# Kernel tuning notes

Measured on AMD Instinct MI355X. Metric: run time of the kernel, lower is better.

## Reference

```python
import jax, jax.numpy as jnp
import numpy as np

B, S, H, NH, FF = 8, 512, 1024, 16, 4096
DK = H // NH


def _ln(x, g, b):
    m = x.mean(-1, keepdims=True)
    v = ((x - m) ** 2).mean(-1, keepdims=True)
    return (x - m) / jnp.sqrt(v + 1e-5) * g + b


def _fwd(x, predicate_pos, attn_bias, attention_mask, atom_graph, variable_graph,
         ln1_g, ln1_b, wq, bq, wk, bk, wv, bv, wo, bo,
         pq_w, pq_b, pk_w, pk_b, pv_w, pv_b, ln2_g, ln2_b, w1, b1, w2, b2):
    b_, s_, h_ = x.shape
    y = _ln(x, ln1_g, ln1_b)
    # ---- self attention (manual MHA with additive bias + mask) ----
    scale = DK ** -0.5
    q = (y @ wq + bq).reshape(b_, s_, NH, DK) * scale
    k = (y @ wk + bk).reshape(b_, s_, NH, DK)
    v = (y @ wv + bv).reshape(b_, s_, NH, DK)
    scores = jnp.einsum('bihd,bjhd->bhij', q, k)
    scores = scores + attn_bias[:, None, :, :] + attention_mask[:, None, :, :]
    att = jax.nn.softmax(scores, axis=-1)
    y_self = jnp.einsum('bhij,bjhd->bihd', att, v).reshape(b_, s_, h_) @ wo + bo
    # ---- path attention (single-head with graph biases) ----
    pscale = h_ ** -0.5
    pq = (y @ pq_w + pq_b) * pscale
    pk = y @ pk_w + pk_b
    pv = y @ pv_w + pv_b
    patt = jnp.einsum('bid,bjd->bij', pq, pk) + atom_graph + variable_graph
    patt = jax.nn.softmax(patt, axis=-1)
    xp = jnp.einsum('bij,bjd->bid', patt, pv)  # [B,S,H]
    # vectorized gather-mean over predicate positions (replaces per-sample loop)
    prev = jnp.concatenate([xp[:, :1], xp[:, :-1]], axis=1)   # xp[i-1]
    nxt = jnp.concatenate([xp[:, 1:], xp[:, -1:]], axis=1)    # xp[i+1]
    a0 = xp[:, 0:2].mean(axis=1, keepdims=True)               # i == 0
    a1 = xp[:, 0:3].mean(axis=1, keepdims=True)               # i == 1
    a2 = (xp + nxt) / 2.0                                     # pos[i-2] == 1
    a3 = (prev + xp + nxt) / 3.0                              # else
    i_arr = jnp.arange(s_)
    pos = (predicate_pos == 1)
    pos_m2 = jnp.pad(pos[:, :-2], ((0, 0), (2, 0)))           # pos[i-2], False for i<2
    atom = jnp.where(pos_m2[..., None], a2, a3)
    atom = jnp.where((i_arr == 1)[None, :, None], a1, atom)
    atom = jnp.where((i_arr == 0)[None, :, None], a0, atom)
    w = pos.astype(xp.dtype)
    path = (atom * w[..., None]).sum(1) / w.sum(1, keepdims=True)  # [B,H]
    y_path = jnp.broadcast_to(path[:, None, :], (b_, s_, h_))
    # ---- combine + residual + FFN ----
    x = x + (y_self + y_path) / 2.0
    y2 = _ln(x, ln2_g, ln2_b)
    hmid = jax.nn.gelu(y2 @ w1 + b1, approximate=False)
    return x + (hmid @ w2 + b2)


def setup_inputs() -> dict:
    key = jax.random.key(0)
    ks = jax.random.split(key, 16)
    def w(k, shape):
        return 0.02 * jax.random.normal(k, shape, dtype=jnp.float32)
    pp = jax.random.randint(ks[0], (B, S), 0, 2, dtype=jnp.int32)
    pp = pp.at[:, 2].set(1).at[:, -1].set(0)  # >=1 predicate; no predicate at last node
    return {
        'x': jax.random.normal(ks[1], (B, S, H), dtype=jnp.float32),
        'predicate_pos': pp,
        'variable_tags': jnp.zeros((B, S), dtype=jnp.int32),
        'attn_bias': 0.1 * jax.random.normal(ks[2], (B, S, S), dtype=jnp.float32),
        'attention_mask': jnp.zeros((B, S, S), dtype=jnp.float32),
        'atom_graph': 0.1 * jax.random.normal(ks[3], (B, S, S), dtype=jnp.float32),
        'variable_graph': 0.1 * jax.random.normal(ks[4], (B, S, S), dtype=jnp.float32),
        'ln1_g': jnp.ones((H,), jnp.float32), 'ln1_b': jnp.zeros((H,), jnp.float32),
        'wq': w(ks[5], (H, H)), 'bq': jnp.zeros((H,), jnp.float32),
        'wk': w(ks[6], (H, H)), 'bk': jnp.zeros((H,), jnp.float32),
        'wv': w(ks[7], (H, H)), 'bv': jnp.zeros((H,), jnp.float32),
        'wo': w(ks[8], (H, H)), 'bo': jnp.zeros((H,), jnp.float32),
        'pq_w': w(ks[9], (H, H)), 'pq_b': jnp.zeros((H,), jnp.float32),
        'pk_w': w(ks[10], (H, H)), 'pk_b': jnp.zeros((H,), jnp.float32),
        'pv_w': w(ks[11], (H, H)), 'pv_b': jnp.zeros((H,), jnp.float32),
        'ln2_g': jnp.ones((H,), jnp.float32), 'ln2_b': jnp.zeros((H,), jnp.float32),
        'w1': w(ks[12], (H, FF)), 'b1': jnp.zeros((FF,), jnp.float32),
        'w2': w(ks[13], (FF, H)), 'b2': jnp.zeros((H,), jnp.float32),
    }


def reference(x, predicate_pos, variable_tags, attn_bias, attention_mask, atom_graph, variable_graph,
              ln1_g, ln1_b, wq, bq, wk, bk, wv, bv, wo, bo,
              pq_w, pq_b, pk_w, pk_b, pv_w, pv_b, ln2_g, ln2_b, w1, b1, w2, b2):
    # variable_tags is unused in the original forward as well
    return _fwd(x, predicate_pos, attn_bias, attention_mask, atom_graph, variable_graph,
                ln1_g, ln1_b, wq, bq, wk, bk, wv, bv, wo, bo,
                pq_w, pq_b, pk_w, pk_b, pv_w, pv_b, ln2_g, ln2_b, w1, b1, w2, b2)
```

## Files before the change

### kernel.cpp

```cpp
#include <hip/hip_runtime.h>
#include <hip/hip_bf16.h>
#include <math.h>


typedef __bf16 bf16x8 __attribute__((ext_vector_type(8)));
typedef float f32x4 __attribute__((ext_vector_type(4)));

__device__ __forceinline__ void async_copy16(void* lds, const void* g) {
  __builtin_amdgcn_global_load_lds(
      (__attribute__((address_space(1))) void*)(void*)g,
      (__attribute__((address_space(3))) void*)lds, 16, 0, 0);
}

#define SB0 __builtin_amdgcn_sched_barrier(0)
#define BARRIER __builtin_amdgcn_s_barrier()

__global__ __launch_bounds__(256) void ln_rows_bf16(
    const float* __restrict__ X, const float* __restrict__ G,
    const float* __restrict__ Bt, __hip_bfloat16* __restrict__ O) {
  long row = blockIdx.x;
  int t = threadIdx.x;
  const float4 xv = ((const float4*)(X + row * 1024))[t];
  float s = xv.x + xv.y + xv.z + xv.w;
  float q = xv.x * xv.x + xv.y * xv.y + xv.z * xv.z + xv.w * xv.w;
#pragma unroll
  for (int o = 32; o; o >>= 1) {
    s += __shfl_xor(s, o);
    q += __shfl_xor(q, o);
  }
  __shared__ float rs[4], rq[4];
  int wid = t >> 6;
  if ((t & 63) == 0) { rs[wid] = s; rq[wid] = q; }
  __syncthreads();
  s = rs[0] + rs[1] + rs[2] + rs[3];
  q = rq[0] + rq[1] + rq[2] + rq[3];
  float mean = s * (1.f / 1024.f);
  float var = q * (1.f / 1024.f) - mean * mean;
  float rstd = rsqrtf(var + 1e-5f);
  const float4 gv = ((const float4*)G)[t];
  const float4 bv = ((const float4*)Bt)[t];
  __hip_bfloat16* o = O + row * 1024 + t * 4;
  o[0] = __float2bfloat16((xv.x - mean) * rstd * gv.x + bv.x);
  o[1] = __float2bfloat16((xv.y - mean) * rstd * gv.y + bv.y);
  o[2] = __float2bfloat16((xv.z - mean) * rstd * gv.z + bv.z);
  o[3] = __float2bfloat16((xv.w - mean) * rstd * gv.w + bv.w);
}

struct PrepJobs {
  const float* in[15];
  __hip_bfloat16* out[15];
  int inLd[15];
  int outLd[15];
  float scale[15];
  const float* bsrc[6];
  float bscale[6];
  float* bias6;
  const float* lnx;
  const float* lng;
  const float* lnb;
  __hip_bfloat16* lno;
};
__global__ __launch_bounds__(256) void prep_weights(PrepJobs p) {
  int j = blockIdx.z;
  int tid = threadIdx.x;
  if (j >= 16) {
    long row = (long)(j - 16) * 1024 + blockIdx.y * 32 + blockIdx.x;
    const float4 xv = ((const float4*)(p.lnx + row * 1024))[tid];
    float s = xv.x + xv.y + xv.z + xv.w;
    float q = xv.x * xv.x + xv.y * xv.y + xv.z * xv.z + xv.w * xv.w;
#pragma unroll
    for (int o = 32; o; o >>= 1) {
      s += __shfl_xor(s, o);
      q += __shfl_xor(q, o);
    }
    __shared__ float rs[4], rq[4];
    int wid = tid >> 6;
    if ((tid & 63) == 0) { rs[wid] = s; rq[wid] = q; }
    __syncthreads();
    s = rs[0] + rs[1] + rs[2] + rs[3];
    q = rq[0] + rq[1] + rq[2] + rq[3];
    float mean = s * (1.f / 1024.f);
    float var = q * (1.f / 1024.f) - mean * mean;
    float rstd = rsqrtf(var + 1e-5f);
    const float4 gv = ((const float4*)p.lng)[tid];
    const float4 bv = ((const float4*)p.lnb)[tid];
    __hip_bfloat16* o = p.lno + row * 1024 + tid * 4;
    o[0] = __float2bfloat16((xv.x - mean) * rstd * gv.x + bv.x);
    o[1] = __float2bfloat16((xv.y - mean) * rstd * gv.y + bv.y);
    o[2] = __float2bfloat16((xv.z - mean) * rstd * gv.z + bv.z);
    o[3] = __float2bfloat16((xv.w - mean) * rstd * gv.w + bv.w);
    return;
  }
  if (j == 15) {
    if (blockIdx.y == 0 && blockIdx.x < 24) {
      int idx = blockIdx.x * 256 + tid;
      int jj = idx >> 10, e = idx & 1023;
      p.bias6[idx] = p.bsrc[jj][e] * p.bscale[jj];
    }
    return;
  }
  __shared__ float t[32][33];
  const float* in = p.in[j];
  __hip_bfloat16* out = p.out[j];
  const int inLd = p.inLd[j], outLd = p.outLd[j];
  const float sc = p.scale[j];
  int c0 = blockIdx.x * 32, r0 = blockIdx.y * 32;
  int lr = tid >> 3, lc = (tid & 7) * 4;
  const float4 v = *(const float4*)&in[(long)(r0 + lr) * inLd + c0 + lc];
  t[lr][lc] = v.x; t[lr][lc + 1] = v.y; t[lr][lc + 2] = v.z; t[lr][lc + 3] = v.w;
  __syncthreads();
  int oc = tid >> 3, orr = (tid & 7) * 4;
  __hip_bfloat16* o = &out[(long)(c0 + oc) * outLd + r0 + orr];
  o[0] = __float2bfloat16(t[orr][oc] * sc);
  o[1] = __float2bfloat16(t[orr + 1][oc] * sc);
  o[2] = __float2bfloat16(t[orr + 2][oc] * sc);
  o[3] = __float2bfloat16(t[orr + 3][oc] * sc);
}

__global__ __launch_bounds__(256) void tconv_vpv(
    const __hip_bfloat16* __restrict__ V, const __hip_bfloat16* __restrict__ PV,
    __hip_bfloat16* __restrict__ VT, __hip_bfloat16* __restrict__ PVT) {
  __shared__ __hip_bfloat16 t[32][34];
  int z = blockIdx.z;
  const __hip_bfloat16* in = (z < 8) ? V : PV;
  __hip_bfloat16* out = (z < 8) ? VT : PVT;
  int bz = z & 7;
  long ibase = (long)bz * 512 * 6144;
  long obase = (long)bz * 512 * 1024;
  int c0 = blockIdx.x * 32, r0 = blockIdx.y * 32;
  int tid = threadIdx.x;
  int lr = tid >> 3, lc = (tid & 7) * 4;
  const __hip_bfloat16* ip = &in[ibase + (long)(r0 + lr) * 6144 + c0 + lc];
  t[lr][lc] = ip[0]; t[lr][lc + 1] = ip[1]; t[lr][lc + 2] = ip[2]; t[lr][lc + 3] = ip[3];
  __syncthreads();
  int oc = tid >> 3, orr = (tid & 7) * 4;
  __hip_bfloat16* o = &out[obase + (long)(c0 + oc) * 512 + r0 + orr];
  o[0] = t[orr][oc];
  o[1] = t[orr + 1][oc];
  o[2] = t[orr + 2][oc];
  o[3] = t[orr + 3][oc];
}

__global__ __launch_bounds__(512, 2) void gemm256(
    const __hip_bfloat16* __restrict__ A, const __hip_bfloat16* __restrict__ Bt,
    const float* __restrict__ bias, void* __restrict__ C, int K, int lda,
    int ldb, int ldc, int act, int obf, long sC) {
  constexpr int ABYTES = 256 * 64;
  constexpr int BBYTES = 128 * 64;
  constexpr int BUF = ABYTES + BBYTES;
  __shared__ char lds[2 * BUF];

  int bx, by;
  {
    int wg = blockIdx.y * gridDim.x + blockIdx.x;
    int gx = gridDim.x, gy = gridDim.y;
    if ((gx & 3) == 0 && (gy & 1) == 0) {
      int cw = gx >> 2, ch = gy >> 1;
      int xcd = wg & 7, idx = wg >> 3;
      bx = (xcd & 3) * cw + idx % cw;
      by = (xcd >> 2) * ch + idx / cw;
    } else {
      bx = blockIdx.x;
      by = blockIdx.y;
    }
  }
  const int m0 = by * 256, n0 = bx * 128;
  const int z = blockIdx.z;
  const long kbase = (long)z * K * 2;

  const int tid = threadIdx.x;
  const int lane = tid & 63, wid = tid >> 6;
  const int wm = wid >> 2, wn = wid & 3;
  const int ll = lane & 15, lh = lane >> 4;

  const char* Ag = (const char*)A;
  const char* Bg = (const char*)Bt;
  const int srow = tid >> 2;
  const int ssw = (srow ^ (srow >> 2)) & 3;
  const int scb = (((tid & 3) ^ ssw) << 4);
  const int sld = (tid & 3) << 4;

  auto stage = [&](char* base, long kb) {
#pragma unroll
    for (int l = 0; l < 2; ++l) {
      int row = l * 128 + srow;
      async_copy16(base + row * 64 + sld,
                   Ag + ((long)(m0 + row) * lda) * 2 + kb + scb);
    }
    async_copy16(base + ABYTES + srow * 64 + sld,
                 Bg + ((long)(n0 + srow) * ldb) * 2 + kb + scb);
  };

  const int rsw = (ll ^ (ll >> 2)) & 3;
  const int ckk = ((lh ^ rsw) << 4);

  f32x4 acc[8][2];
#pragma unroll
  for (int m = 0; m < 8; ++m)
#pragma unroll
    for (int n = 0; n < 2; ++n) acc[m][n] = (f32x4){0.f, 0.f, 0.f, 0.f};

  const int nt = K >> 5;
  stage(lds, kbase);

  for (int t = 0; t < nt; ++t) {
    const int bt = t & 1;
    const char* Ab = lds + bt * BUF;
    const char* Bb = Ab + ABYTES;
    char* nb = lds + (bt ^ 1) * BUF;

    SB0; BARRIER; SB0;
    if (t + 1 < nt) {
      stage(nb, kbase + (long)(t + 1) * 64);
      asm volatile("s_waitcnt vmcnt(3)" ::: "memory");
    } else {
      asm volatile("s_waitcnt vmcnt(0)" ::: "memory");
    }
    SB0; BARRIER; SB0;

    bf16x8 bf[2];
#pragma unroll
    for (int n = 0; n < 2; ++n)
      bf[n] = *(const bf16x8*)(Bb + (wn * 32 + n * 16 + ll) * 64 + ckk);
    bf16x8 af[4];
#pragma unroll
    for (int m = 0; m < 4; ++m)
      af[m] = *(const bf16x8*)(Ab + (wm * 128 + m * 16 + ll) * 64 + ckk);
    __builtin_amdgcn_s_setprio(1);
#pragma unroll
    for (int m = 0; m < 4; ++m)
#pragma unroll
      for (int n = 0; n < 2; ++n)
        acc[m][n] = __builtin_amdgcn_mfma_f32_16x16x32_bf16(af[m], bf[n],
                                                            acc[m][n], 0, 0, 0);
    __builtin_amdgcn_s_setprio(0);
#pragma unroll
    for (int m = 0; m < 4; ++m)
      af[m] = *(const bf16x8*)(Ab + (wm * 128 + (m + 4) * 16 + ll) * 64 + ckk);
    __builtin_amdgcn_s_setprio(1);
#pragma unroll
    for (int m = 0; m < 4; ++m)
#pragma unroll
      for (int n = 0; n < 2; ++n)
        acc[m + 4][n] = __builtin_amdgcn_mfma_f32_16x16x32_bf16(
            af[m], bf[n], acc[m + 4][n], 0, 0, 0);
    __builtin_amdgcn_s_setprio(0);
  }

#pragma unroll
  for (int m = 0; m < 8; ++m) {
    int row = m0 + wm * 128 + m * 16 + lh * 4;
#pragma unroll
    for (int n = 0; n < 2; ++n) {
      int col = n0 + wn * 32 + n * 16 + ll;
      float bs = bias ? bias[col] : 0.f;
#pragma unroll
      for (int r = 0; r < 4; ++r) {
        float v = acc[m][n][r] + bs;
        if (act) v = v * 0.5f * (1.f + erff(v * 0.70710678118f));
        long cidx = (long)z * sC + (long)(row + r) * ldc + col;
        if (obf)
          ((__hip_bfloat16*)C)[cidx] = __float2bfloat16(v);
        else
          ((float*)C)[cidx] = v;
      }
    }
  }
}

__global__ __launch_bounds__(256) void ffn2_reduce(
    const float* __restrict__ P, const float* __restrict__ X2,
    const float* __restrict__ b2, float* __restrict__ OUT) {
  int i = blockIdx.x * 256 + threadIdx.x;
  const long SP = 4194304;
  float4 a = ((const float4*)P)[i];
  float4 b = ((const float4*)(P + SP))[i];
  float4 c = ((const float4*)(P + 2 * SP))[i];
  float4 d = ((const float4*)(P + 3 * SP))[i];
  float4 xr = ((const float4*)X2)[i];
  const float4 bb = *(const float4*)(b2 + ((i & 255) * 4));
  float4 o;
  o.x = a.x + b.x + c.x + d.x + xr.x + bb.x;
  o.y = a.y + b.y + c.y + d.y + xr.y + bb.y;
  o.z = a.z + b.z + c.z + d.z + xr.z + bb.z;
  o.w = a.w + b.w + c.w + d.w + xr.w + bb.w;
  ((float4*)OUT)[i] = o;
}

__global__ __launch_bounds__(256) void gemm_bf16_nt(
    const __hip_bfloat16* __restrict__ A, const __hip_bfloat16* __restrict__ Bt,
    const float* __restrict__ bias, const float* __restrict__ E1,
    const float* __restrict__ E2, void* __restrict__ C, int K, int lda,
    int ldb, int ldc, long sA, long sB, long sC, long sE, float alpha, int act,
    int obf, int pbc, int ksplit, long sSplit) {
  __shared__ unsigned short AsU[2][128 * 32];
  __shared__ unsigned short BsU[2][128 * 32];
  const int tid = threadIdx.x;
  const int lane = tid & 63, wave = tid >> 6;
  const int wr = wave >> 1, wc = wave & 1;

  int nwg = gridDim.x * gridDim.y;
  int wg = blockIdx.y * gridDim.x + blockIdx.x;
  int bx = blockIdx.x, by = blockIdx.y;
  if ((nwg & 7) == 0) {
    int cpx = nwg >> 3;
    int sw = (wg & 7) * cpx + (wg >> 3);
    bx = sw % gridDim.x;
    by = sw / gridDim.x;
  }
  const int m0 = by * 128, n0 = bx * 128;
  const int bz = blockIdx.z / ksplit;
  const int sk = blockIdx.z % ksplit;
  if (sk != 0) { bias = nullptr; E1 = nullptr; E2 = nullptr; }
  const int kcol0 = sk * K;
  const char* Ab = (const char*)(A + (long)bz * sA);
  const char* Bb = (const char*)(Bt + (long)bz * sB);

  f32x4 acc[4][4];
#pragma unroll
  for (int m = 0; m < 4; ++m)
#pragma unroll
    for (int n = 0; n < 4; ++n) acc[m][n] = (f32x4){0.f, 0.f, 0.f, 0.f};

  const int srow = tid >> 2;
  const int scol = (tid & 3) * 16;
  const int wbase = (tid >> 6) * 1024;

  auto stage = [&](int buf, int k0) {
    int kk = kcol0 + k0;
#pragma unroll
    for (int i = 0; i < 2; ++i) {
      async_copy16((char*)AsU[buf] + i * 4096 + wbase,
                   Ab + ((long)(m0 + i * 64 + srow) * lda + kk) * 2 + scol);
      async_copy16((char*)BsU[buf] + i * 4096 + wbase,
                   Bb + ((long)(n0 + i * 64 + srow) * ldb + kk) * 2 + scol);
    }
  };

  const int ntk = K >> 5;
  stage(0, 0);

  for (int t = 0; t < ntk; ++t) {
    const int bt = t & 1;
    SB0; BARRIER; SB0;
    if (t + 1 < ntk) {
      stage(bt ^ 1, (t + 1) * 32);
      asm volatile("s_waitcnt vmcnt(4)" ::: "memory");
    } else {
      asm volatile("s_waitcnt vmcnt(0)" ::: "memory");
    }
    SB0; BARRIER; SB0;

    const int koff = (lane >> 4) * 8;
    bf16x8 a[4], b[4];
#pragma unroll
    for (int m = 0; m < 4; ++m)
      a[m] = *(const bf16x8*)&AsU[bt][(wr * 64 + m * 16 + (lane & 15)) * 32 +
                                      koff];
#pragma unroll
    for (int n = 0; n < 4; ++n)
      b[n] = *(const bf16x8*)&BsU[bt][(wc * 64 + n * 16 + (lane & 15)) * 32 +
                                      koff];
    __builtin_amdgcn_s_setprio(1);
#pragma unroll
    for (int m = 0; m < 4; ++m)
#pragma unroll
      for (int n = 0; n < 4; ++n)
        acc[m][n] = __builtin_amdgcn_mfma_f32_16x16x32_bf16(a[m], b[n],
                                                            acc[m][n], 0, 0, 0);
    __builtin_amdgcn_s_setprio(0);
  }

#pragma unroll
  for (int m = 0; m < 4; ++m) {
    int row = m0 + wr * 64 + m * 16 + (lane >> 4) * 4;
#pragma unroll
    for (int n = 0; n < 4; ++n) {
      int col = n0 + wc * 64 + n * 16 + (lane & 15);
      float bs = bias ? bias[col] : 0.f;
#pragma unroll
      for (int r = 0; r < 4; ++r) {
        float v = (acc[m][n][r] + bs) * alpha;
        if (pbc) {
          v = E1[(long)(row + r) * ldc + col] +
              0.5f * (v + E2[(long)((row + r) >> 9) * 1024 + col]);
        } else {
          long eidx = (long)bz * sE + (long)(row + r) * ldc + col;
          if (E1) v += E1[eidx];
          if (E2) v += E2[eidx];
        }
        if (act) v = v * 0.5f * (1.f + erff(v * 0.70710678118f));
        long cidx = (long)bz * sC + (long)sk * sSplit +
                    (long)(row + r) * ldc + col;
        if (obf)
          ((__hip_bfloat16*)C)[cidx] = __float2bfloat16(v);
        else
          ((float*)C)[cidx] = v;
      }
    }
  }
}

__global__ __launch_bounds__(256) void attn_mfma(
    const __hip_bfloat16* __restrict__ Q, const __hip_bfloat16* __restrict__ K,
    const __hip_bfloat16* __restrict__ VT, const float* __restrict__ BiasP,
    const float* __restrict__ MaskP, __hip_bfloat16* __restrict__ O,
    int ldqk) {
  __shared__ __hip_bfloat16 P[32][520];
  __shared__ float red[2][32][4];
  const int it = blockIdx.x, h = blockIdx.y, b = blockIdx.z;
  const int i0 = it * 32;
  const int tid = threadIdx.x;
  const int lane = tid & 63, w = tid >> 6;
  const int lh = lane >> 4, ll = lane & 15;

  const long qkb = (long)b * 512 * ldqk + h * 64;

  bf16x8 a[2][2];
#pragma unroll
  for (int m = 0; m < 2; ++m)
#pragma unroll
    for (int ks = 0; ks < 2; ++ks)
      a[m][ks] = *(const bf16x8*)&Q[qkb + (long)(i0 + m * 16 + ll) * ldqk +
                                    ks * 32 + lh * 8];

  f32x4 acc[2][8];
#pragma unroll
  for (int m = 0; m < 2; ++m)
#pragma unroll
    for (int n = 0; n < 8; ++n) acc[m][n] = (f32x4){0.f, 0.f, 0.f, 0.f};

#pragma unroll
  for (int n = 0; n < 8; ++n) {
    const __hip_bfloat16* kp =
        &K[qkb + (long)(w * 128 + n * 16 + ll) * ldqk + lh * 8];
    bf16x8 b0 = *(const bf16x8*)&kp[0];
    bf16x8 b1 = *(const bf16x8*)&kp[32];
#pragma unroll
    for (int m = 0; m < 2; ++m) {
      acc[m][n] =
          __builtin_amdgcn_mfma_f32_16x16x32_bf16(a[m][0], b0, acc[m][n], 0, 0, 0);
      acc[m][n] =
          __builtin_amdgcn_mfma_f32_16x16x32_bf16(a[m][1], b1, acc[m][n], 0, 0, 0);
    }
  }

  const long bmo = ((long)b * 512 + i0) * 512 + w * 128;
#pragma unroll
  for (int m = 0; m < 2; ++m)
#pragma unroll
    for (int r = 0; r < 4; ++r) {
      int row = m * 16 + lh * 4 + r;
#pragma unroll
      for (int n = 0; n < 8; ++n) {
        long gi = bmo + (long)row * 512 + n * 16 + ll;
        acc[m][n][r] += BiasP[gi] + MaskP[gi];
      }
    }

  float rmax[2][4];
#pragma unroll
  for (int m = 0; m < 2; ++m)
#pragma unroll
    for (int r = 0; r < 4; ++r) {
      float v = acc[m][0][r];
#pragma unroll
      for (int n = 1; n < 8; ++n) v = fmaxf(v, acc[m][n][r]);
#pragma unroll
      for (int o = 1; o < 16; o <<= 1) v = fmaxf(v, __shfl_xor(v, o));
      rmax[m][r] = v;
    }
  if (ll == 0) {
#pragma unroll
    for (int m = 0; m < 2; ++m)
#pragma unroll
      for (int r = 0; r < 4; ++r) red[0][m * 16 + lh * 4 + r][w] = rmax[m][r];
  }
  __syncthreads();
#pragma unroll
  for (int m = 0; m < 2; ++m)
#pragma unroll
    for (int r = 0; r < 4; ++r) {
      const float* p = red[0][m * 16 + lh * 4 + r];
      rmax[m][r] = fmaxf(fmaxf(p[0], p[1]), fmaxf(p[2], p[3]));
    }
  float rsum[2][4];
#pragma unroll
  for (int m = 0; m < 2; ++m)
#pragma unroll
    for (int r = 0; r < 4; ++r) {
      float s = 0.f;
#pragma unroll
      for (int n = 0; n < 8; ++n) {
        float e = __expf(acc[m][n][r] - rmax[m][r]);
        acc[m][n][r] = e;
        s += e;
      }
#pragma unroll
      for (int o = 1; o < 16; o <<= 1) s += __shfl_xor(s, o);
      rsum[m][r] = s;
    }
  if (ll == 0) {
#pragma unroll
    for (int m = 0; m < 2; ++m)
#pragma unroll
      for (int r = 0; r < 4; ++r) red[1][m * 16 + lh * 4 + r][w] = rsum[m][r];
  }
  __syncthreads();
#pragma unroll
  for (int m = 0; m < 2; ++m)
#pragma unroll
    for (int r = 0; r < 4; ++r) {
      const float* p = red[1][m * 16 + lh * 4 + r];
      float inv = 1.f / (p[0] + p[1] + p[2] + p[3]);
      int row = m * 16 + lh * 4 + r;
#pragma unroll
      for (int n = 0; n < 8; ++n)
        P[row][w * 128 + n * 16 + ll] = __float2bfloat16(acc[m][n][r] * inv);
    }
  __syncthreads();

  const long vtb = ((long)b * 1024 + h * 64) * 512;
  const long ob = (long)b * 512 * 1024 + h * 64;
  const int mw = (w >> 1) * 16, nw = (w & 1) * 32;
  f32x4 oacc[2];
  oacc[0] = (f32x4){0.f, 0.f, 0.f, 0.f};
  oacc[1] = (f32x4){0.f, 0.f, 0.f, 0.f};
#pragma unroll
  for (int ks = 0; ks < 16; ++ks) {
    int k0 = ks * 32;
    bf16x8 pa = *(const bf16x8*)&P[mw + ll][k0 + lh * 8];
#pragma unroll
    for (int nf = 0; nf < 2; ++nf) {
      bf16x8 vb = *(const bf16x8*)&VT[vtb + (long)(nw + nf * 16 + ll) * 512 +
                                      k0 + lh * 8];
      oacc[nf] =
          __builtin_amdgcn_mfma_f32_16x16x32_bf16(pa, vb, oacc[nf], 0, 0, 0);
    }
  }
#pragma unroll
  for (int nf = 0; nf < 2; ++nf)
#pragma unroll
    for (int r = 0; r < 4; ++r)
      O[ob + (long)(i0 + mw + lh * 4 + r) * 1024 + nw + nf * 16 + ll] =
          __float2bfloat16(oacc[nf][r]);
}

__global__ __launch_bounds__(256) void softmax_rows2(
    const float* __restrict__ P0, const float* __restrict__ P1,
    __hip_bfloat16* __restrict__ Ob) {
  const float* r0 = P0 + (long)blockIdx.x * 512;
  const float* r1 = P1 + (long)blockIdx.x * 512;
  __hip_bfloat16* orow = Ob + (long)blockIdx.x * 512;
  int t = threadIdx.x;
  float v0 = r0[t] + r1[t], v1 = r0[t + 256] + r1[t + 256];
  float m = fmaxf(v0, v1);
#pragma unroll
  for (int o = 32; o; o >>= 1) m = fmaxf(m, __shfl_xor(m, o));
  __shared__ float red[8];
  int wid = t >> 6, lane = t & 63;
  if (!lane) red[wid] = m;
  __syncthreads();
  m = fmaxf(fmaxf(red[0], red[1]), fmaxf(red[2], red[3]));
  float e0 = __expf(v0 - m), e1 = __expf(v1 - m);
  float s = e0 + e1;
#pragma unroll
  for (int o = 32; o; o >>= 1) s += __shfl_xor(s, o);
  if (!lane) red[4 + wid] = s;
  __syncthreads();
  s = red[4] + red[5] + red[6] + red[7];
  float inv = 1.f / s;
  orow[t] = __float2bfloat16(e0 * inv);
  orow[t + 256] = __float2bfloat16(e1 * inv);
}

__global__ __launch_bounds__(256) void path_partial(
    const float* __restrict__ xp, const int* __restrict__ pp,
    float* __restrict__ PP, float* __restrict__ WS) {
  int b = blockIdx.x, hc = blockIdx.y, ic = blockIdx.z;
  int h = hc * 256 + threadIdx.x;
  const int* ppb = pp + b * 512;
  const float* xb = xp + (long)b * 512 * 1024;
  int iA = ic * 64, iB = iA + 64;
  float acc = 0.f;
  for (int i = iA; i < iB; ++i) {
    if (ppb[i] != 1) continue;
    float cur = xb[(long)i * 1024 + h];
    float a;
    if (i == 0) {
      a = 0.5f * (cur + xb[1024 + h]);
    } else if (i == 1) {
      a = (xb[h] + cur + xb[2 * 1024 + h]) * (1.f / 3.f);
    } else {
      int inx = (i + 1 < 512) ? i + 1 : 511;
      float nx = xb[(long)inx * 1024 + h];
      if (ppb[i - 2] == 1) {
        a = 0.5f * (cur + nx);
      } else {
        a = (xb[(long)(i - 1) * 1024 + h] + cur + nx) * (1.f / 3.f);
      }
    }
    acc += a;
  }
  PP[((long)b * 8 + ic) * 1024 + h] = acc;
  if (hc == 0 && threadIdx.x == 0) {
    float c = 0.f;
    for (int i = iA; i < iB; ++i) c += (ppb[i] == 1) ? 1.f : 0.f;
    WS[b * 8 + ic] = c;
  }
}

__global__ __launch_bounds__(256) void path_finalize(
    const float* __restrict__ PP, const float* __restrict__ WS,
    float* __restrict__ PATH) {
  int b = blockIdx.x;
  int h = blockIdx.y * 256 + threadIdx.x;
  float s = 0.f, w = 0.f;
#pragma unroll
  for (int ic = 0; ic < 8; ++ic) {
    s += PP[((long)b * 8 + ic) * 1024 + h];
    w += WS[b * 8 + ic];
  }
  PATH[b * 1024 + h] = s / w;
}

extern "C" void kernel_launch(void* const* d_in, const int* in_sizes, int n_in,
                              void* d_out, int out_size, void* d_ws,
                              size_t ws_size, hipStream_t stream) {
  const float* x = (const float*)d_in[0];
  const int* pp = (const int*)d_in[1];
  const float* abias = (const float*)d_in[3];
  const float* amask = (const float*)d_in[4];
  const float* agraph = (const float*)d_in[5];
  const float* vgraph = (const float*)d_in[6];
  const float* ln1g = (const float*)d_in[7];
  const float* ln1b = (const float*)d_in[8];
  const float* wq = (const float*)d_in[9];
  const float* bq = (const float*)d_in[10];
  const float* wk = (const float*)d_in[11];
  const float* bk = (const float*)d_in[12];
  const float* wv = (const float*)d_in[13];
  const float* bv = (const float*)d_in[14];
  const float* wo = (const float*)d_in[15];
  const float* bo = (const float*)d_in[16];
  const float* pqw = (const float*)d_in[17];
  const float* pqb = (const float*)d_in[18];
  const float* pkw = (const float*)d_in[19];
  const float* pkb = (const float*)d_in[20];
  const float* pvw = (const float*)d_in[21];
  const float* pvb = (const float*)d_in[22];
  const float* ln2g = (const float*)d_in[23];
  const float* ln2b = (const float*)d_in[24];
  const float* w1 = (const float*)d_in[25];
  const float* b1 = (const float*)d_in[26];
  const float* w2 = (const float*)d_in[27];
  const float* b2 = (const float*)d_in[28];

  char* wsb = (char*)d_ws;
  auto Ybf = (__hip_bfloat16*)(wsb);
  auto QKV = (__hip_bfloat16*)(wsb + (8l << 20));
  auto VTb = (__hip_bfloat16*)(wsb + (56l << 20));
  auto PVT = (__hip_bfloat16*)(wsb + (64l << 20));
  auto ATTb = (__hip_bfloat16*)(wsb + (72l << 20));
  auto PATTb = (__hip_bfloat16*)(wsb + (88l << 20));
  auto PATTf = (float*)(wsb + (92l << 20));
  auto XP = (float*)(wsb + (92l << 20));
  auto WALL = (__hip_bfloat16*)(wsb + (108l << 20));
  auto WOT = (__hip_bfloat16*)(wsb + (120l << 20));
  auto W1T = (__hip_bfloat16*)(wsb + (122l << 20));
  auto bias6 = (float*)(wsb + (130l << 20));
  auto PPart = (float*)(wsb + (131l << 20));
  auto WSp = (float*)(wsb + (132l << 20));
  auto PATH = (float*)(wsb + (133l << 20));
  auto X2 = (float*)(wsb + (24l << 20));
  auto HMID = (__hip_bfloat16*)(wsb + (40l << 20));
  auto PART = (float*)(wsb + (92l << 20));
  auto W2T = (__hip_bfloat16*)(wsb + (156l << 20));
  __hip_bfloat16* Y2b = Ybf;
  float* OUT = (float*)d_out;

  const float qscale = 0.125f;
  const float pscale = 0.03125f;
  const long S2 = 512l * 512;
  const long SQ = 512l * 6144;
  const long SPLT = 8l * S2;

  __hip_bfloat16* Qp = QKV;
  __hip_bfloat16* Kp = QKV + 1024;
  __hip_bfloat16* Vp = QKV + 2048;
  __hip_bfloat16* PQp = QKV + 3072;
  __hip_bfloat16* PKp = QKV + 4096;
  __hip_bfloat16* PVp = QKV + 5120;

  PrepJobs pj;
  pj.in[0] = wq;  pj.out[0] = WALL;               pj.inLd[0] = 1024; pj.outLd[0] = 1024; pj.scale[0] = qscale;
  pj.in[1] = wk;  pj.out[1] = WALL + 1024 * 1024; pj.inLd[1] = 1024; pj.outLd[1] = 1024; pj.scale[1] = 1.f;
  pj.in[2] = wv;  pj.out[2] = WALL + 2048 * 1024; pj.inLd[2] = 1024; pj.outLd[2] = 1024; pj.scale[2] = 1.f;
  pj.in[3] = pqw; pj.out[3] = WALL + 3072 * 1024; pj.inLd[3] = 1024; pj.outLd[3] = 1024; pj.scale[3] = pscale;
  pj.in[4] = pkw; pj.out[4] = WALL + 4096 * 1024; pj.inLd[4] = 1024; pj.outLd[4] = 1024; pj.scale[4] = 1.f;
  pj.in[5] = pvw; pj.out[5] = WALL + 5120 * 1024; pj.inLd[5] = 1024; pj.outLd[5] = 1024; pj.scale[5] = 1.f;
  pj.in[6] = wo;  pj.out[6] = WOT;                pj.inLd[6] = 1024; pj.outLd[6] = 1024; pj.scale[6] = 1.f;
  for (int j = 0; j < 4; ++j) {
    pj.in[7 + j] = w1 + j * 1024;
    pj.out[7 + j] = W1T + (long)j * 1024 * 1024;
    pj.inLd[7 + j] = 4096;
    pj.outLd[7 + j] = 1024;
    pj.scale[7 + j] = 1.f;
  }
  for (int j = 0; j < 4; ++j) {
    pj.in[11 + j] = w2 + (long)j * 1024 * 1024;
    pj.out[11 + j] = W2T + j * 1024;
    pj.inLd[11 + j] = 1024;
    pj.outLd[11 + j] = 4096;
    pj.scale[11 + j] = 1.f;
  }
  pj.bsrc[0] = bq;  pj.bscale[0] = qscale;
  pj.bsrc[1] = bk;  pj.bscale[1] = 1.f;
  pj.bsrc[2] = bv;  pj.bscale[2] = 1.f;
  pj.bsrc[3] = pqb; pj.bscale[3] = pscale;
  pj.bsrc[4] = pkb; pj.bscale[4] = 1.f;
  pj.bsrc[5] = pvb; pj.bscale[5] = 1.f;
  pj.bias6 = bias6;
  pj.lnx = x; pj.lng = ln1g; pj.lnb = ln1b; pj.lno = Ybf;
  prep_weights<<<dim3(32, 32, 20), 256, 0, stream>>>(pj);

  gemm256<<<dim3(48, 16, 1), 512, 0, stream>>>(
      Ybf, WALL, bias6, QKV, 1024, 1024, 1024, 6144, 0, 1, 0);

  tconv_vpv<<<dim3(32, 16, 16), 256, 0, stream>>>(Vp, PVp, VTb, PVT);

  gemm_bf16_nt<<<dim3(4, 4, 16), 256, 0, stream>>>(
      PQp, PKp, nullptr, agraph, vgraph, PATTf, 512, 6144, 6144, 512, SQ, SQ,
      S2, S2, 1.f, 0, 0, 0, 2, SPLT);
  softmax_rows2<<<4096, 256, 0, stream>>>(PATTf, PATTf + SPLT, PATTb);

  attn_mfma<<<dim3(16, 16, 8), 256, 0, stream>>>(Qp, Kp, VTb, abias, amask,
                                                 ATTb, 6144);

  gemm_bf16_nt<<<dim3(8, 4, 8), 256, 0, stream>>>(
      PATTb, PVT, nullptr, nullptr, nullptr, XP, 512, 512, 512, 1024, S2,
      512l * 1024, 512l * 1024, 0, 1.f, 0, 0, 0, 1, 0);

  path_partial<<<dim3(8, 4, 8), 256, 0, stream>>>(XP, pp, PPart, WSp);
  path_finalize<<<dim3(8, 4), 256, 0, stream>>>(PPart, WSp, PATH);

  gemm_bf16_nt<<<dim3(8, 32, 1), 256, 0, stream>>>(
      ATTb, WOT, bo, x, PATH, X2, 1024, 1024, 1024, 1024, 0, 0, 0, 0, 1.f, 0,
      0, 1, 1, 0);

  ln_rows_bf16<<<4096, 256, 0, stream>>>(X2, ln2g, ln2b, Y2b);

  gemm256<<<dim3(32, 16, 1), 512, 0, stream>>>(
      Y2b, W1T, b1, HMID, 1024, 1024, 1024, 4096, 1, 1, 0);

  gemm256<<<dim3(8, 16, 4), 512, 0, stream>>>(
      HMID, W2T, nullptr, PART, 1024, 4096, 4096, 1024, 0, 0, 4194304);

  ffn2_reduce<<<4096, 256, 0, stream>>>(PART, X2, b2, OUT);
}
```

Measured before the change: 438.1 us.

## Merge independent kernels into combined launches to cut launch count

Puts the V/PV transpose and the path score GEMM into one launch, choosing the branch by blockIdx.z. It also puts self-attention and the path softmax into a second combined launch. These pairs are independent, so each launch can run both workloads at once and there are fewer launches and fewer idle gaps between them. In exchange, the combined kernels hold both branches' shared memory and register use, which may lower occupancy, and some blocks in the padded grid exit immediately.

```diff
diff --git a/kernel.cpp b/kernel.cpp
--- a/kernel.cpp
+++ b/kernel.cpp
@@ -117,30 +117,6 @@
   o[3] = __float2bfloat16(t[orr + 3][oc] * sc);
 }
 
-__global__ __launch_bounds__(256) void tconv_vpv(
-    const __hip_bfloat16* __restrict__ V, const __hip_bfloat16* __restrict__ PV,
-    __hip_bfloat16* __restrict__ VT, __hip_bfloat16* __restrict__ PVT) {
-  __shared__ __hip_bfloat16 t[32][34];
-  int z = blockIdx.z;
-  const __hip_bfloat16* in = (z < 8) ? V : PV;
-  __hip_bfloat16* out = (z < 8) ? VT : PVT;
-  int bz = z & 7;
-  long ibase = (long)bz * 512 * 6144;
-  long obase = (long)bz * 512 * 1024;
-  int c0 = blockIdx.x * 32, r0 = blockIdx.y * 32;
-  int tid = threadIdx.x;
-  int lr = tid >> 3, lc = (tid & 7) * 4;
-  const __hip_bfloat16* ip = &in[ibase + (long)(r0 + lr) * 6144 + c0 + lc];
-  t[lr][lc] = ip[0]; t[lr][lc + 1] = ip[1]; t[lr][lc + 2] = ip[2]; t[lr][lc + 3] = ip[3];
-  __syncthreads();
-  int oc = tid >> 3, orr = (tid & 7) * 4;
-  __hip_bfloat16* o = &out[obase + (long)(c0 + oc) * 512 + r0 + orr];
-  o[0] = t[orr][oc];
-  o[1] = t[orr + 1][oc];
-  o[2] = t[orr + 2][oc];
-  o[3] = t[orr + 3][oc];
-}
-
 __global__ __launch_bounds__(512, 2) void gemm256(
     const __hip_bfloat16* __restrict__ A, const __hip_bfloat16* __restrict__ Bt,
     const float* __restrict__ bias, void* __restrict__ C, int K, int lda,
@@ -287,30 +263,30 @@
   ((float4*)OUT)[i] = o;
 }
 
-__global__ __launch_bounds__(256) void gemm_bf16_nt(
+__device__ __forceinline__ void gemm_nt_dev(
     const __hip_bfloat16* __restrict__ A, const __hip_bfloat16* __restrict__ Bt,
-    const float* __restrict__ bias, const float* __restrict__ E1,
-    const float* __restrict__ E2, void* __restrict__ C, int K, int lda,
-    int ldb, int ldc, long sA, long sB, long sC, long sE, float alpha, int act,
-    int obf, int pbc, int ksplit, long sSplit) {
+    const float* bias, const float* E1, const float* E2, void* __restrict__ C,
+    int K, int lda, int ldb, int ldc, long sA, long sB, long sC, long sE,
+    float alpha, int act, int obf, int pbc, int ksplit, long sSplit,
+    int bxRaw, int byRaw, int bzRaw, int gx, int gy) {
   __shared__ unsigned short AsU[2][128 * 32];
   __shared__ unsigned short BsU[2][128 * 32];
   const int tid = threadIdx.x;
   const int lane = tid & 63, wave = tid >> 6;
   const int wr = wave >> 1, wc = wave & 1;
 
-  int nwg = gridDim.x * gridDim.y;
-  int wg = blockIdx.y * gridDim.x + blockIdx.x;
-  int bx = blockIdx.x, by = blockIdx.y;
+  int nwg = gx * gy;
+  int wg = byRaw * gx + bxRaw;
+  int bx = bxRaw, by = byRaw;
   if ((nwg & 7) == 0) {
     int cpx = nwg >> 3;
     int sw = (wg & 7) * cpx + (wg >> 3);
-    bx = sw % gridDim.x;
-    by = sw / gridDim.x;
+    bx = sw % gx;
+    by = sw / gx;
   }
   const int m0 = by * 128, n0 = bx * 128;
-  const int bz = blockIdx.z / ksplit;
-  const int sk = blockIdx.z % ksplit;
+  const int bz = bzRaw / ksplit;
+  const int sk = bzRaw % ksplit;
   if (sk != 0) { bias = nullptr; E1 = nullptr; E2 = nullptr; }
   const int kcol0 = sk * K;
   const char* Ab = (const char*)(A + (long)bz * sA);
@@ -401,14 +377,24 @@
   }
 }
 
-__global__ __launch_bounds__(256) void attn_mfma(
-    const __hip_bfloat16* __restrict__ Q, const __hip_bfloat16* __restrict__ K,
+__global__ __launch_bounds__(256) void gemm_bf16_nt(
+    const __hip_bfloat16* A, const __hip_bfloat16* Bt, const float* bias,
+    const float* E1, const float* E2, void* C, int K, int lda, int ldb,
+    int ldc, long sA, long sB, long sC, long sE, float alpha, int act,
+    int obf, int pbc, int ksplit, long sSplit) {
+  gemm_nt_dev(A, Bt, bias, E1, E2, C, K, lda, ldb, ldc, sA, sB, sC, sE, alpha,
+              act, obf, pbc, ksplit, sSplit, blockIdx.x, blockIdx.y,
+              blockIdx.z, gridDim.x, gridDim.y);
+}
+
+__device__ __forceinline__ void attn_dev(
+    int it, int h, int b, const __hip_bfloat16* __restrict__ Q,
+    const __hip_bfloat16* __restrict__ K,
     const __hip_bfloat16* __restrict__ VT, const float* __restrict__ BiasP,
     const float* __restrict__ MaskP, __hip_bfloat16* __restrict__ O,
     int ldqk) {
   __shared__ __hip_bfloat16 P[32][520];
   __shared__ float red[2][32][4];
-  const int it = blockIdx.x, h = blockIdx.y, b = blockIdx.z;
   const int i0 = it * 32;
   const int tid = threadIdx.x;
   const int lane = tid & 63, w = tid >> 6;
@@ -546,32 +532,84 @@
           __float2bfloat16(oacc[nf][r]);
 }
 
-__global__ __launch_bounds__(256) void softmax_rows2(
-    const float* __restrict__ P0, const float* __restrict__ P1,
-    __hip_bfloat16* __restrict__ Ob) {
-  const float* r0 = P0 + (long)blockIdx.x * 512;
-  const float* r1 = P1 + (long)blockIdx.x * 512;
-  __hip_bfloat16* orow = Ob + (long)blockIdx.x * 512;
+__device__ __forceinline__ void softmax_dev(long row_i,
+                                            const float* __restrict__ P0,
+                                            const float* __restrict__ P1,
+                                            __hip_bfloat16* __restrict__ Ob) {
+  const float* r0 = P0 + row_i * 512;
+  const float* r1 = P1 + row_i * 512;
+  __hip_bfloat16* orow = Ob + row_i * 512;
   int t = threadIdx.x;
   float v0 = r0[t] + r1[t], v1 = r0[t + 256] + r1[t + 256];
   float m = fmaxf(v0, v1);
 #pragma unroll
   for (int o = 32; o; o >>= 1) m = fmaxf(m, __shfl_xor(m, o));
-  __shared__ float red[8];
+  __shared__ float sred[8];
   int wid = t >> 6, lane = t & 63;
-  if (!lane) red[wid] = m;
+  if (!lane) sred[wid] = m;
   __syncthreads();
-  m = fmaxf(fmaxf(red[0], red[1]), fmaxf(red[2], red[3]));
+  m = fmaxf(fmaxf(sred[0], sred[1]), fmaxf(sred[2], sred[3]));
   float e0 = __expf(v0 - m), e1 = __expf(v1 - m);
   float s = e0 + e1;
 #pragma unroll
   for (int o = 32; o; o >>= 1) s += __shfl_xor(s, o);
-  if (!lane) red[4 + wid] = s;
+  if (!lane) sred[4 + wid] = s;
   __syncthreads();
-  s = red[4] + red[5] + red[6] + red[7];
+  s = sred[4] + sred[5] + sred[6] + sred[7];
   float inv = 1.f / s;
   orow[t] = __float2bfloat16(e0 * inv);
   orow[t + 256] = __float2bfloat16(e1 * inv);
+}
+
+__global__ __launch_bounds__(256) void tconv_path(
+    const __hip_bfloat16* __restrict__ V, const __hip_bfloat16* __restrict__ PV,
+    __hip_bfloat16* __restrict__ VT, __hip_bfloat16* __restrict__ PVT,
+    const __hip_bfloat16* PQ, const __hip_bfloat16* PK,
+    const float* agraph, const float* vgraph, float* PATTf, long SQ, long S2,
+    long SPLT) {
+  int z = blockIdx.z;
+  if (z < 16) {
+    __shared__ __hip_bfloat16 t[32][34];
+    const __hip_bfloat16* in = (z < 8) ? V : PV;
+    __hip_bfloat16* out = (z < 8) ? VT : PVT;
+    int bz = z & 7;
+    long ibase = (long)bz * 512 * 6144;
+    long obase = (long)bz * 512 * 1024;
+    int c0 = blockIdx.x * 32, r0 = blockIdx.y * 32;
+    int tid = threadIdx.x;
+    int lr = tid >> 3, lc = (tid & 7) * 4;
+    const __hip_bfloat16* ip = &in[ibase + (long)(r0 + lr) * 6144 + c0 + lc];
+    t[lr][lc] = ip[0]; t[lr][lc + 1] = ip[1];
+    t[lr][lc + 2] = ip[2]; t[lr][lc + 3] = ip[3];
+    __syncthreads();
+    int oc = tid >> 3, orr = (tid & 7) * 4;
+    __hip_bfloat16* o = &out[obase + (long)(c0 + oc) * 512 + r0 + orr];
+    o[0] = t[orr][oc];
+    o[1] = t[orr + 1][oc];
+    o[2] = t[orr + 2][oc];
+    o[3] = t[orr + 3][oc];
+    return;
+  }
+  int bid2 = blockIdx.y * 32 + blockIdx.x;
+  if (bid2 >= 256) return;
+  gemm_nt_dev(PQ, PK, nullptr, agraph, vgraph, PATTf, 512, 6144, 6144, 512,
+              SQ, SQ, S2, S2, 1.f, 0, 0, 0, 2, SPLT, bid2 & 3,
+              (bid2 >> 2) & 3, bid2 >> 4, 4, 4);
+}
+
+__global__ __launch_bounds__(256) void attn_softmax(
+    const __hip_bfloat16* __restrict__ Q, const __hip_bfloat16* __restrict__ K,
+    const __hip_bfloat16* __restrict__ VT, const float* __restrict__ BiasP,
+    const float* __restrict__ MaskP, __hip_bfloat16* __restrict__ O, int ldqk,
+    const float* __restrict__ P0, const float* __restrict__ P1,
+    __hip_bfloat16* __restrict__ Ob) {
+  int z = blockIdx.z;
+  if (z < 8) {
+    attn_dev(blockIdx.x, blockIdx.y, z, Q, K, VT, BiasP, MaskP, O, ldqk);
+    return;
+  }
+  long row = (long)(z - 8) * 256 + blockIdx.y * 16 + blockIdx.x;
+  softmax_dev(row, P0, P1, Ob);
 }
 
 __global__ __launch_bounds__(256) void path_partial(
@@ -727,15 +765,11 @@
   gemm256<<<dim3(48, 16, 1), 512, 0, stream>>>(
       Ybf, WALL, bias6, QKV, 1024, 1024, 1024, 6144, 0, 1, 0);
 
-  tconv_vpv<<<dim3(32, 16, 16), 256, 0, stream>>>(Vp, PVp, VTb, PVT);
-
-  gemm_bf16_nt<<<dim3(4, 4, 16), 256, 0, stream>>>(
-      PQp, PKp, nullptr, agraph, vgraph, PATTf, 512, 6144, 6144, 512, SQ, SQ,
-      S2, S2, 1.f, 0, 0, 0, 2, SPLT);
-  softmax_rows2<<<4096, 256, 0, stream>>>(PATTf, PATTf + SPLT, PATTb);
-
-  attn_mfma<<<dim3(16, 16, 8), 256, 0, stream>>>(Qp, Kp, VTb, abias, amask,
-                                                 ATTb, 6144);
+  tconv_path<<<dim3(32, 16, 17), 256, 0, stream>>>(
+      Vp, PVp, VTb, PVT, PQp, PKp, agraph, vgraph, PATTf, SQ, S2, SPLT);
+
+  attn_softmax<<<dim3(16, 16, 24), 256, 0, stream>>>(
+      Qp, Kp, VTb, abias, amask, ATTb, 6144, PATTf, PATTf + SPLT, PATTb);
 
   gemm_bf16_nt<<<dim3(8, 4, 8), 256, 0, stream>>>(
       PATTb, PVT, nullptr, nullptr, nullptr, XP, 512, 512, 512, 1024, S2,
```

Result: slower. 456.7 us (+4.2%).
